# Kernel optimization log

Hardware: AMD Instinct MI355X
Metric: run time of the kernel (lower is better)

Reference implementation:

```python
import jax, jax.numpy as jnp
import numpy as np

IMG = 640
STRIDES = (8, 16, 32)
A = 5            # anchors per level
NC = 80          # num classes
IOU_TH = 0.5
NEG_RATIO = 1.0


def make_priors():
    scales = [1.0, 1.5, 2.0, 2.5, 3.0]
    out = []
    for s in STRIDES:
        f = IMG // s
        ys, xs = np.meshgrid(np.arange(f), np.arange(f), indexing='ij')
        cx = ((xs + 0.5) / f).ravel()
        cy = ((ys + 0.5) / f).ravel()
        for sc in scales:  # anchor-major to match merge_features (A, h, w) order
            wh = min(sc * 4.0 * s / IMG, 1.0)
            out.append(np.stack([cx, cy, np.full_like(cx, wh), np.full_like(cx, wh)], 1))
    return np.concatenate(out, 0).astype(np.float32)  # [42000, 4] cxcywh


def merge_features(feats):
    outs = []
    for feat in feats:
        n, c, h, w = feat.shape
        f = feat.reshape(n, A, c // A, h, w).transpose(0, 1, 3, 4, 2)
        outs.append(f.reshape(n, A * h * w, c // A))
    return jnp.concatenate(outs, axis=1)  # [n, M, 85]


def box_iou_cxcywh(a, b):
    # a [T,4], b [M,4] (cx,cy,w,h) -> IoU [T,M]
    a1 = jnp.concatenate([a[:, :2] - a[:, 2:] / 2, a[:, :2] + a[:, 2:] / 2], -1)
    b1 = jnp.concatenate([b[:, :2] - b[:, 2:] / 2, b[:, :2] + b[:, 2:] / 2], -1)
    tl = jnp.maximum(a1[:, None, :2], b1[None, :, :2])
    br = jnp.minimum(a1[:, None, 2:], b1[None, :, 2:])
    wh = jnp.clip(br - tl, 0.0)
    inter = wh[..., 0] * wh[..., 1]
    area_a = a[:, 2] * a[:, 3]
    area_b = b[:, 2] * b[:, 3]
    return inter / (area_a[:, None] + area_b[None, :] - inter + 1e-9)


def build_targets(targets, priors, batch):
    ious = box_iou_cxcywh(targets[:, 2:6], priors)  # [Nt, M]
    Nt, M = ious.shape
    img_ids = targets[:, 0].astype(jnp.int32)

    def per_image(i):
        valid = img_ids == i  # [Nt]
        iv = jnp.where(valid[:, None], ious, -1.0)
        best_gt_overlap = iv.max(0)            # [M]
        best_gt_idx = iv.argmax(0)             # [M]
        best_prior_idx = iv.argmax(1)          # [Nt]
        # torch: index_fill_(1) then sequential best_gt_overlap[best_prior_idx[j]] = j
        local_j = (jnp.cumsum(valid.astype(jnp.int32)) - 1).astype(jnp.float32)
        scat_idx = jnp.where(valid, best_prior_idx, M)  # drop invalid rows
        best_gt_overlap = best_gt_overlap.at[scat_idx].set(local_j, mode='drop')
        bbox = targets[best_gt_idx, 2:6]
        clss = targets[best_gt_idx, 1] + 1.0
        clss = jnp.where(best_gt_overlap < IOU_TH, 0.0, clss)
        t_xy = (bbox[:, :2] - priors[:, :2]) / priors[:, 2:]
        t_wh = jnp.log(bbox[:, 2:] / priors[:, 2:])
        return t_xy, t_wh, clss

    return jax.vmap(per_image)(jnp.arange(batch))  # [B,M,2],[B,M,2],[B,M]


def _smooth_l1(x):
    ax = jnp.abs(x)
    return jnp.where(ax < 1.0, 0.5 * ax * ax, ax - 0.5)


def compute_loss(preds, priors, targets):
    n, m, _ = preds.shape
    t_xy, t_wh, t_cls = build_targets(targets, priors, n)
    pos = t_cls > 0
    posf = pos.astype(preds.dtype)
    num_pos = posf.sum()

    # lbox: smooth L1 on xy and wh over positives (mean over pos*2 elements each)
    den2 = jnp.maximum(num_pos * 2.0, 1.0)
    lbox = (_smooth_l1(preds[..., 0:2] - t_xy) * posf[..., None]).sum() / den2 \
         + (_smooth_l1(preds[..., 2:4] - t_wh) * posf[..., None]).sum() / den2

    # lcls: cross entropy over positives, labels = t_cls - 1
    labels = jnp.clip(t_cls.astype(jnp.int32) - 1, 0, NC - 1)
    logz = jax.nn.log_softmax(preds[..., 5:], axis=-1)
    ce = -jnp.take_along_axis(logz, labels[..., None], axis=-1)[..., 0]
    lcls = (ce * posf).sum() / jnp.maximum(num_pos, 1.0)

    # hard negative mining (no grad): double argsort rank trick
    obj = preds[..., 4]
    loss_c = jax.lax.stop_gradient(-jax.nn.log_sigmoid(obj))
    loss_c = jnp.where(pos, 0.0, loss_c)
    order = jnp.argsort(-loss_c, axis=-1)
    rank = jnp.argsort(order, axis=-1)
    num_neg = jnp.minimum(NEG_RATIO * num_pos, m - num_pos)
    neg = rank.astype(preds.dtype) < num_neg
    sel = (pos | neg).astype(preds.dtype)

    # lobj: BCE-with-logits over pos|neg
    z = posf
    bce = jnp.maximum(obj, 0.0) - obj * z + jnp.log1p(jnp.exp(-jnp.abs(obj)))
    lobj = (bce * sel).sum() / jnp.maximum(sel.sum(), 1.0)

    loss = lbox + lcls + lobj
    return jnp.stack([loss, lbox, lobj, lcls])


def setup_inputs() -> dict:
    key = jax.random.key(0)
    ks = jax.random.split(key, 6)
    feat0 = jax.random.normal(ks[0], (8, 425, 80, 80), jnp.float32)
    feat1 = jax.random.normal(ks[1], (8, 425, 40, 40), jnp.float32)
    feat2 = jax.random.normal(ks[2], (8, 425, 20, 20), jnp.float32)
    B, T = 8, 20
    img = jnp.repeat(jnp.arange(B, dtype=jnp.float32), T)
    cls = jax.random.randint(ks[3], (B * T,), 0, NC).astype(jnp.float32)
    cxcy = jax.random.uniform(ks[4], (B * T, 2), minval=0.2, maxval=0.8)
    wh = jax.random.uniform(ks[5], (B * T, 2), minval=0.05, maxval=0.3)
    targets = jnp.concatenate([img[:, None], cls[:, None], cxcy, wh], 1)
    priors = jnp.asarray(make_priors())
    return {"feat0": feat0, "feat1": feat1, "feat2": feat2,
            "targets": targets, "priors": priors}


def reference(feat0, feat1, feat2, targets, priors):
    preds = merge_features([feat0, feat1, feat2])  # [8, 42000, 85]
    return compute_loss(preds, priors, targets)    # [loss, lbox, lobj, lcls]
```

## Files before the change

### kernel.cpp

```cpp
#include <hip/hip_runtime.h>
#include <math.h>

#define MTOT 42000
#define NB 8
#define NCLS 80
#define CAP_LIST 4096
#define MAXT 256
#define NT_MAX 2048
#define GX_MAIN 165
#define NBLK_MAIN (GX_MAIN*NB)
#define NCH 32
#define CS 1313

#define O_OVR 0
#define O_GIX (O_OVR + NB*MTOT*4)
#define O_OBJ (O_GIX + NB*MTOT*4)
#define O_LSC (O_OBJ + NB*MTOT*4)
#define O_BCE (O_LSC + NB*MTOT*4)
#define O_LST (O_BCE + NB*MTOT*4)
#define O_LJ  (O_LST + NB*MAXT*4)
#define O_CNT (O_LJ + NT_MAX*4)
#define O_BPP (((O_CNT + 64 + 7)/8)*8)
#define O_PA  (O_BPP + NT_MAX*NCH*8)
#define O_PN  (O_PA + NBLK_MAIN*16)
#define O_P2  (O_PN + NBLK_MAIN*4)
#define O_BINL (O_P2 + NBLK_MAIN*8)
#define O_HA  (((O_BINL + NB*CAP_LIST*2*4 + 255)/256)*256)
#define O_HB  (O_HA + NB*256*4)
#define O_ACC (O_HB + NB*256*4)
#define O_ACCI (O_ACC + 64)
#define O_ZEND (O_ACCI + 128)
#define ZWORDS ((O_ZEND - O_HA)/4)
#define ZBLK ((ZWORDS + 255)/256)

__device__ __forceinline__ float iou_cxcywh(float acx,float acy,float aw,float ah,
                                            float bcx,float bcy,float bw,float bh){
  float ax0=acx-aw*0.5f, ay0=acy-ah*0.5f, ax1=acx+aw*0.5f, ay1=acy+ah*0.5f;
  float bx0=bcx-bw*0.5f, by0=bcy-bh*0.5f, bx1=bcx+bw*0.5f, by1=bcy+bh*0.5f;
  float tlx=fmaxf(ax0,bx0), tly=fmaxf(ay0,by0);
  float brx=fminf(ax1,bx1), bry=fminf(ay1,by1);
  float wx=fmaxf(brx-tlx,0.f), wy=fmaxf(bry-tly,0.f);
  float inter=wx*wy;
  return inter/(aw*ah+bw*bh-inter+1e-9f);
}

__device__ __forceinline__ float sl1(float x){
  float ax=fabsf(x); return ax<1.f ? 0.5f*ax*ax : ax-0.5f;
}

__device__ __forceinline__ void feat_base(const float* f0,const float* f1,const float* f2,
                                          int i,int m,const float** basep,int* hwp){
  const float* fp; int hw, loc;
  if(m<32000){ fp=f0; hw=6400; loc=m; }
  else if(m<40000){ fp=f1; hw=1600; loc=m-32000; }
  else { fp=f2; hw=400; loc=m-40000; }
  int a=loc/hw, p=loc-a*hw;
  *basep = fp + (size_t)(i*425 + a*85)*(size_t)hw + p;
  *hwp = hw;
}

__device__ __forceinline__ void fine_scan(const unsigned* hb,int ca,int kres,int* bs_out,int* r_out){
  if(ca==0x7fffffff){ *bs_out=0x7fffffff; *r_out=0; return; }
  int run=0, bs=-1, r=0;
  for(int f=255;f>=0;f--){
    int cb=(int)hb[f];
    if(run<kres && run+cb>=kres){ bs=(ca<<8)|f; r=kres-run; break; }
    run+=cb;
  }
  if(bs<0){ bs=(ca<<8); r=kres-run; }
  *bs_out=bs; *r_out=r;
}

__global__ void k_init(const float* __restrict__ tg, int nt, int* __restrict__ list,
                       int* __restrict__ cnt, int* __restrict__ lj,
                       unsigned* __restrict__ zbase){
  int bx=blockIdx.x, tid=threadIdx.x;
  if(bx<ZBLK){
    int w=bx*256+tid;
    if(w<ZWORDS) zbase[w]=0u;
    return;
  }
  if(bx==ZBLK && tid<NB){
    int c=0;
    for(int q=0;q<nt;q++) if((int)tg[q*6]==tid) c++;
    cnt[tid]=c;
  }
  int t=(bx-ZBLK)*256+tid;
  if(t>=nt) return;
  int img=(int)tg[t*6];
  int j=0;
  for(int q=0;q<t;q++) if((int)tg[q*6]==img) j++;
  lj[t]=j;
  if(img>=0 && img<NB && j<MAXT) list[img*MAXT+j]=t;
}

__global__ void k_big1(const float* __restrict__ f0,const float* __restrict__ f1,const float* __restrict__ f2,
                       const float* __restrict__ tg,const float* __restrict__ priors,
                       const int* __restrict__ list,const int* __restrict__ cnt,int nt,
                       float* __restrict__ ovr,int* __restrict__ gix,
                       float* __restrict__ objc,unsigned long long* __restrict__ bpp){
  __shared__ float st[MAXT*6];
  __shared__ int sidx[MAXT];
  __shared__ unsigned long long su[256];
  int b=blockIdx.x, tid=threadIdx.x;
  if(b<NBLK_MAIN){
    int i=b/GX_MAIN, cb=b-(b/GX_MAIN)*GX_MAIN;
    int n=min(cnt[i],MAXT);
    for(int j=tid;j<n;j+=256){
      int t=list[i*MAXT+j];
      sidx[j]=t;
      #pragma unroll
      for(int q=0;q<6;q++) st[j*6+q]=tg[t*6+q];
    }
    __syncthreads();
    int m=cb*256+tid;
    if(m>=MTOT) return;
    float4 pr=((const float4*)priors)[m];
    float maxv=-1.f; int bi=0;
    for(int j=0;j<n;j++){
      float v=iou_cxcywh(st[j*6+2],st[j*6+3],st[j*6+4],st[j*6+5],pr.x,pr.y,pr.z,pr.w);
      if(v>maxv){ maxv=v; bi=sidx[j]; }
    }
    ovr[i*MTOT+m]=maxv; gix[i*MTOT+m]=bi;
  } else if(b<2*NBLK_MAIN){
    int idx=b-NBLK_MAIN;
    int i=idx/GX_MAIN, cb=idx-(idx/GX_MAIN)*GX_MAIN;
    int m=cb*256+tid;
    if(m>=MTOT) return;
    const float* base; int hw;
    feat_base(f0,f1,f2,i,m,&base,&hw);
    objc[i*MTOT+m]=base[(size_t)4*hw];
  } else {
    int idx=b-2*NBLK_MAIN;
    int t=idx/NCH, c=idx-(idx/NCH)*NCH;
    float acx=tg[t*6+2],acy=tg[t*6+3],aw=tg[t*6+4],ah=tg[t*6+5];
    int m0=c*CS, m1=min(m0+CS,MTOT);
    float bv=-1.f; int bm=0;
    for(int m=m0+tid;m<m1;m+=256){
      float4 pr=((const float4*)priors)[m];
      float v=iou_cxcywh(acx,acy,aw,ah,pr.x,pr.y,pr.z,pr.w);
      if(v>bv){ bv=v; bm=m; }
    }
    unsigned long long p=(bv<0.f)?0ull
        :(((unsigned long long)__float_as_uint(bv))<<32)|(unsigned)(~bm);
    su[tid]=p;
    __syncthreads();
    for(int o=128;o>0;o>>=1){
      if(tid<o){ if(su[tid+o]>su[tid]) su[tid]=su[tid+o]; }
      __syncthreads();
    }
    if(tid==0) bpp[(size_t)t*NCH+c]=su[0];
  }
}

__global__ void k_bpsc(const float* __restrict__ tg,int nt,
                       const unsigned long long* __restrict__ bpp,
                       const int* __restrict__ lj,float* __restrict__ ovr){
  __shared__ int tbp[NT_MAX];
  __shared__ int timg[NT_MAX];
  int tid=threadIdx.x;
  for(int t=tid;t<nt;t+=256){
    unsigned long long best=0ull;
    const unsigned long long* pp=&bpp[(size_t)t*NCH];
    for(int c=0;c<NCH;c++){ unsigned long long v=pp[c]; if(v>best) best=v; }
    int bm=~((unsigned)(best&0xFFFFFFFFull));
    tbp[t]=min(max(bm,0),MTOT-1);
    timg[t]=(int)tg[t*6];
  }
  __syncthreads();
  for(int t=tid;t<nt;t+=256){
    int img=timg[t];
    if(img<0||img>=NB) continue;
    int myp=tbp[t];
    bool last=true;
    for(int q=t+1;q<nt;q++) if(timg[q]==img&&tbp[q]==myp){ last=false; break; }
    if(last) ovr[img*MTOT+myp]=(float)lj[t];
  }
}

__global__ void k_lc(const float* __restrict__ tg,const float* __restrict__ objc,
                     const float* __restrict__ ovr,const int* __restrict__ gix,int nt,
                     float* __restrict__ lsc,float* __restrict__ bcearr,
                     unsigned* __restrict__ histA,int* __restrict__ partN){
  __shared__ unsigned h[256];
  __shared__ int snp[4];
  int tid=threadIdx.x, lane=tid&63, wid=tid>>6;
  h[tid]=0u;
  __syncthreads();
  int i=blockIdx.y;
  int m=blockIdx.x*256+tid;
  int npos=0;
  if(m<MTOT){
    int gid=i*MTOT+m;
    float ov=ovr[gid];
    int gi=min(max(gix[gid],0),nt-1);
    float tc=tg[gi*6+1]+1.f;
    bool pos=(ov>=0.5f)&&(tc>0.f);
    float obj=objc[gid];
    float sp=log1pf(expf(-fabsf(obj)));
    float bce=fmaxf(obj,0.f)-(pos?obj:0.f)+sp;
    float lc=pos?0.f:(fmaxf(-obj,0.f)+sp);
    lsc[gid]=lc; bcearr[gid]=bce;
    atomicAdd(&h[__float_as_uint(lc)>>24],1u);
    npos=pos?1:0;
  }
  #pragma unroll
  for(int o=32;o>0;o>>=1) npos+=__shfl_xor(npos,o);
  if(lane==0) snp[wid]=npos;
  __syncthreads();
  unsigned hc=h[tid];
  if(hc) atomicAdd(&histA[i*256+tid],hc);
  if(tid==0) partN[blockIdx.y*GX_MAIN+blockIdx.x]=snp[0]+snp[1]+snp[2]+snp[3];
}

__global__ void k_redscanA(const int* __restrict__ partN,const unsigned* __restrict__ histA,
                           int* __restrict__ acci){
  __shared__ int an[256];
  __shared__ unsigned h[256];
  int t=threadIdx.x, b=blockIdx.x;
  int n=0;
  for(int e=t;e<NBLK_MAIN;e+=256) n+=partN[e];
  an[t]=n;
  __syncthreads();
  for(int o=128;o>0;o>>=1){ if(t<o) an[t]+=an[t+o]; __syncthreads(); }
  int np=an[0];
  if(b==0&&t==0) acci[0]=np;
  h[t]=histA[b*256+t];
  __syncthreads();
  if(t==0){
    int kk=min(np,MTOT-np);
    if(kk<=0){ acci[2+b]=0x7fffffff; acci[10+b]=0; }
    else{
      int run=0, ca=-1, kres=0;
      for(int c2=255;c2>=0;c2--){
        int cbn=(int)h[c2];
        if(run<kk&&run+cbn>=kk){ ca=c2; kres=kk-run; break; }
        run+=cbn;
      }
      if(ca<0){ ca=0; kres=kk-run; }
      acci[2+b]=ca; acci[10+b]=kres;
    }
  }
}

__global__ void k_big2(const float* __restrict__ f0,const float* __restrict__ f1,const float* __restrict__ f2,
                       const float* __restrict__ tg,const float* __restrict__ priors,
                       const float* __restrict__ ovr,const int* __restrict__ gix,
                       const float* __restrict__ lsc,const float* __restrict__ bcearr,
                       const int* __restrict__ acci,int nt,
                       unsigned* __restrict__ histB,float4* __restrict__ partA){
  __shared__ unsigned h[256];
  __shared__ float rA[4],rB[4],rC[4],rD[4];
  int b=blockIdx.x, tid=threadIdx.x, lane=tid&63, wid=tid>>6;
  if(b<NBLK_MAIN){
    h[tid]=0u;
    __syncthreads();
    int i=b/GX_MAIN, cb=b-(b/GX_MAIN)*GX_MAIN;
    int ca=acci[2+i];
    int m=cb*256+tid;
    if(m<MTOT && ca!=0x7fffffff){
      unsigned u=__float_as_uint(lsc[i*MTOT+m]);
      if((int)(u>>24)==ca) atomicAdd(&h[(u>>16)&0xFF],1u);
    }
    __syncthreads();
    unsigned c=h[tid];
    if(c) atomicAdd(&histB[i*256+tid],c);
  } else {
    int idx=b-NBLK_MAIN;
    int i=idx/GX_MAIN, cb=idx-(idx/GX_MAIN)*GX_MAIN;
    int m=cb*256+tid;
    bool valid=(m<MTOT);
    float lxy=0.f,lwh=0.f,bcep=0.f,wce=0.f;
    bool pos=false; int gi=0;
    if(valid){
      int gid=i*MTOT+m;
      float ov=ovr[gid];
      gi=min(max(gix[gid],0),nt-1);
      float tc=tg[gi*6+1]+1.f;
      pos=(ov>=0.5f)&&(tc>0.f);
      if(pos){
        const float* base; int hw;
        feat_base(f0,f1,f2,i,m,&base,&hw);
        bcep=bcearr[gid];
        float4 pr=((const float4*)priors)[m];
        float bx=tg[gi*6+2],by=tg[gi*6+3],bw=tg[gi*6+4],bh=tg[gi*6+5];
        float tx=(bx-pr.x)/pr.z, ty=(by-pr.y)/pr.w;
        float tw=logf(bw/pr.z), th=logf(bh/pr.w);
        lxy=sl1(base[0]-tx)+sl1(base[(size_t)hw]-ty);
        lwh=sl1(base[(size_t)2*hw]-tw)+sl1(base[(size_t)3*hw]-th);
      }
    }
    unsigned long long mask=__ballot(valid&&pos);
    while(mask){
      int s=__ffsll(mask)-1;
      mask&=mask-1;
      int m_s=__shfl(m,s);
      int gi_s=__shfl(gi,s);
      const float* bs2; int hws;
      feat_base(f0,f1,f2,i,m_s,&bs2,&hws);
      int label=(int)(tg[gi_s*6+1]+1.f)-1;
      label=min(NCLS-1,max(0,label));
      float v0=bs2[(size_t)(5+lane)*hws];
      float v1=(lane<16)?bs2[(size_t)(69+lane)*hws]:-3.0e38f;
      float mx=fmaxf(v0,v1);
      #pragma unroll
      for(int o=32;o>0;o>>=1) mx=fmaxf(mx,__shfl_xor(mx,o));
      float se=expf(v0-mx)+((lane<16)?expf(v1-mx):0.f);
      float xl=((lane==label)?v0:0.f)+((lane<16&&lane+64==label)?v1:0.f);
      #pragma unroll
      for(int o=32;o>0;o>>=1){ se+=__shfl_xor(se,o); xl+=__shfl_xor(xl,o); }
      wce+=logf(se)+mx-xl;
    }
    #pragma unroll
    for(int o=32;o>0;o>>=1){
      lxy+=__shfl_xor(lxy,o); lwh+=__shfl_xor(lwh,o); bcep+=__shfl_xor(bcep,o);
    }
    if(lane==0){ rA[wid]=lxy; rB[wid]=lwh; rC[wid]=wce; rD[wid]=bcep; }
    __syncthreads();
    if(tid==0)
      partA[idx]=make_float4(rA[0]+rA[1]+rA[2]+rA[3], rB[0]+rB[1]+rB[2]+rB[3],
                             rC[0]+rC[1]+rC[2]+rC[3], rD[0]+rD[1]+rD[2]+rD[3]);
  }
}

__global__ void k_select(const float* __restrict__ lsc,const float* __restrict__ bcearr,
                         const unsigned* __restrict__ histB,
                         int* __restrict__ acci,float2* __restrict__ part2,
                         int* __restrict__ binlist){
  __shared__ unsigned hb[256];
  __shared__ int sbs;
  __shared__ float ss[4]; __shared__ float sc[4];
  int tid=threadIdx.x, lane=tid&63, wid=tid>>6;
  int i=blockIdx.y;
  int ca=acci[2+i], kres=acci[10+i];
  hb[tid]=(ca==0x7fffffff)?0u:histB[i*256+tid];
  __syncthreads();
  if(tid==0){ int bs,r; fine_scan(hb,ca,kres,&bs,&r); sbs=bs; }
  __syncthreads();
  int bs_=sbs;
  int m=blockIdx.x*256+tid;
  float s=0.f, c=0.f;
  if(m<MTOT){
    int gid=i*MTOT+m;
    unsigned u=__float_as_uint(lsc[gid]);
    int bin=(int)(u>>16);
    if(bin>bs_){ s=bcearr[gid]; c=1.f; }
    else if(bin==bs_){
      int idx=atomicAdd(&acci[18+i],1);
      if(idx<CAP_LIST){
        binlist[((size_t)i*CAP_LIST+idx)*2  ]=(int)u;
        binlist[((size_t)i*CAP_LIST+idx)*2+1]=gid;
      }
    }
  }
  #pragma unroll
  for(int o=32;o>0;o>>=1){ s+=__shfl_xor(s,o); c+=__shfl_xor(c,o); }
  if(lane==0){ ss[wid]=s; sc[wid]=c; }
  __syncthreads();
  if(tid==0) part2[blockIdx.y*gridDim.x+blockIdx.x]=make_float2(ss[0]+ss[1]+ss[2]+ss[3], sc[0]+sc[1]+sc[2]+sc[3]);
}

__global__ void k_ties(const float* __restrict__ bcearr,int* __restrict__ acci,
                       float* __restrict__ accf,const int* __restrict__ binlist,
                       const unsigned* __restrict__ histB){
  __shared__ unsigned hb[256];
  __shared__ int sbs, sr;
  int i=blockIdx.x, tid=threadIdx.x;
  int ca=acci[2+i], kres=acci[10+i];
  hb[tid]=(ca==0x7fffffff)?0u:histB[i*256+tid];
  __syncthreads();
  if(tid==0){ int bs,r; fine_scan(hb,ca,kres,&bs,&r); sbs=bs; sr=r; }
  __syncthreads();
  if(sbs==0x7fffffff) return;
  int n=min(acci[18+i],CAP_LIST);
  int r=sr;
  for(int e=tid;e<n;e+=blockDim.x){
    unsigned ue=(unsigned)binlist[((size_t)i*CAP_LIST+e)*2];
    int ge=binlist[((size_t)i*CAP_LIST+e)*2+1];
    int rank=0;
    for(int q=0;q<n;q++){
      unsigned uq=(unsigned)binlist[((size_t)i*CAP_LIST+q)*2];
      int gq=binlist[((size_t)i*CAP_LIST+q)*2+1];
      rank += ((uq>ue)||(uq==ue&&gq<ge))?1:0;
    }
    if(rank<r){
      atomicAdd(&accf[5], bcearr[ge]);
      atomicAdd(&acci[1], 1);
    }
  }
}

__global__ void k_final(const float4* __restrict__ partA,const float2* __restrict__ part2,
                        const float* __restrict__ accf,const int* __restrict__ acci,
                        float* __restrict__ out){
  __shared__ float a0[256],a1[256],a2[256],a3[256],s0[256],s1[256];
  int tid=threadIdx.x;
  float x=0,y=0,z=0,w=0,ns=0,nc=0;
  for(int e=tid;e<NBLK_MAIN;e+=256){
    float4 p=partA[e]; x+=p.x; y+=p.y; z+=p.z; w+=p.w;
    float2 q=part2[e]; ns+=q.x; nc+=q.y;
  }
  a0[tid]=x; a1[tid]=y; a2[tid]=z; a3[tid]=w; s0[tid]=ns; s1[tid]=nc;
  __syncthreads();
  for(int o=128;o>0;o>>=1){
    if(tid<o){
      a0[tid]+=a0[tid+o]; a1[tid]+=a1[tid+o]; a2[tid]+=a2[tid+o]; a3[tid]+=a3[tid+o];
      s0[tid]+=s0[tid+o]; s1[tid]+=s1[tid+o];
    }
    __syncthreads();
  }
  if(tid==0){
    float negsum=s0[0]+accf[5];
    float negcnt=s1[0]+(float)acci[1];
    int np=acci[0];
    float npf=(float)np;
    float den2=fmaxf(2.f*npf,1.f);
    float lbox=a0[0]/den2+a1[0]/den2;
    float lcls=a2[0]/fmaxf(npf,1.f);
    float selc=npf+negcnt;
    float lobj=(a3[0]+negsum)/fmaxf(selc,1.f);
    out[0]=lbox+lcls+lobj;
    out[1]=lbox;
    out[2]=lobj;
    out[3]=lcls;
  }
}

extern "C" void kernel_launch(void* const* d_in, const int* in_sizes, int n_in,
                              void* d_out, int out_size, void* d_ws, size_t ws_size,
                              hipStream_t stream) {
  const float* f0=(const float*)d_in[0];
  const float* f1=(const float*)d_in[1];
  const float* f2=(const float*)d_in[2];
  const float* tg=(const float*)d_in[3];
  const float* priors=(const float*)d_in[4];
  int nt = in_sizes[3]/6;
  if(nt>NT_MAX) nt=NT_MAX;
  if(nt<1) nt=1;

  char* ws=(char*)d_ws;
  float*    ovr    =(float*)   (ws+O_OVR);
  int*      gix    =(int*)     (ws+O_GIX);
  float*    objc   =(float*)   (ws+O_OBJ);
  float*    lsc    =(float*)   (ws+O_LSC);
  float*    bcearr =(float*)   (ws+O_BCE);
  int*      list   =(int*)     (ws+O_LST);
  int*      lj     =(int*)     (ws+O_LJ);
  int*      cnt    =(int*)     (ws+O_CNT);
  unsigned long long* bpp=(unsigned long long*)(ws+O_BPP);
  float4*   partA  =(float4*)  (ws+O_PA);
  int*      partN  =(int*)     (ws+O_PN);
  float2*   part2  =(float2*)  (ws+O_P2);
  int*      binlist=(int*)     (ws+O_BINL);
  unsigned* histA  =(unsigned*)(ws+O_HA);
  unsigned* histB  =(unsigned*)(ws+O_HB);
  float*    accf   =(float*)   (ws+O_ACC);
  int*      acci   =(int*)     (ws+O_ACCI);
  unsigned* zbase  =(unsigned*)(ws+O_HA);

  int ntb=(nt+255)/256;
  k_init<<<ZBLK+ntb,256,0,stream>>>(tg,nt,list,cnt,lj,zbase);
  k_big1<<<2*NBLK_MAIN+nt*NCH,256,0,stream>>>(f0,f1,f2,tg,priors,list,cnt,nt,ovr,gix,objc,bpp);
  k_bpsc<<<1,256,0,stream>>>(tg,nt,bpp,lj,ovr);
  dim3 gm(GX_MAIN, NB);
  k_lc<<<gm,256,0,stream>>>(tg,objc,ovr,gix,nt,lsc,bcearr,histA,partN);
  k_redscanA<<<NB,256,0,stream>>>(partN,histA,acci);
  k_big2<<<2*NBLK_MAIN,256,0,stream>>>(f0,f1,f2,tg,priors,ovr,gix,lsc,bcearr,acci,nt,histB,partA);
  k_select<<<gm,256,0,stream>>>(lsc,bcearr,histB,acci,part2,binlist);
  k_ties<<<NB,256,0,stream>>>(bcearr,acci,accf,binlist,histB);
  k_final<<<1,256,0,stream>>>(partA,part2,accf,acci,(float*)d_out);
}
```

Before: 138.3 us.

## Fuse init into main IoU kernel, filter targets by image inline, stage tie list in LDS

Merges the init kernel (zeroing, per-target local index) into the big matching kernel, which removes one launch and the per-image list/count dependency. Each prior-matching block now scans all targets in shared-memory chunks and skips targets from other images. The best-prior search uses 8 larger chunks per target instead of 32, giving fewer blocks but more work each. k_ties stages up to 2048 bin-list entries in LDS so the O(n^2) rank loop reads shared memory instead of global memory. The trade-off is that every prior block now iterates over all targets rather than only its image's targets.

```diff
diff --git a/kernel.cpp b/kernel.cpp
--- a/kernel.cpp
+++ b/kernel.cpp
@@ -9,19 +9,18 @@
 #define NT_MAX 2048
 #define GX_MAIN 165
 #define NBLK_MAIN (GX_MAIN*NB)
-#define NCH 32
-#define CS 1313
+#define NCHB 8
+#define CSB 5250
+#define TCH 512
 
 #define O_OVR 0
 #define O_GIX (O_OVR + NB*MTOT*4)
 #define O_OBJ (O_GIX + NB*MTOT*4)
 #define O_LSC (O_OBJ + NB*MTOT*4)
 #define O_BCE (O_LSC + NB*MTOT*4)
-#define O_LST (O_BCE + NB*MTOT*4)
-#define O_LJ  (O_LST + NB*MAXT*4)
-#define O_CNT (O_LJ + NT_MAX*4)
-#define O_BPP (((O_CNT + 64 + 7)/8)*8)
-#define O_PA  (O_BPP + NT_MAX*NCH*8)
+#define O_LJ  (O_BCE + NB*MTOT*4)
+#define O_BPP (((O_LJ + NT_MAX*4 + 7)/8)*8)
+#define O_PA  (O_BPP + NT_MAX*NCHB*8)
 #define O_PN  (O_PA + NBLK_MAIN*16)
 #define O_P2  (O_PN + NBLK_MAIN*4)
 #define O_BINL (O_P2 + NBLK_MAIN*8)
@@ -71,59 +70,56 @@
   *bs_out=bs; *r_out=r;
 }
 
-__global__ void k_init(const float* __restrict__ tg, int nt, int* __restrict__ list,
-                       int* __restrict__ cnt, int* __restrict__ lj,
-                       unsigned* __restrict__ zbase){
-  int bx=blockIdx.x, tid=threadIdx.x;
-  if(bx<ZBLK){
-    int w=bx*256+tid;
+__global__ void k_big0(const float* __restrict__ f0,const float* __restrict__ f1,const float* __restrict__ f2,
+                       const float* __restrict__ tg,const float* __restrict__ priors,
+                       int nt,int b0,int b1,int b2,
+                       int* __restrict__ lj,unsigned* __restrict__ zbase,
+                       float* __restrict__ ovr,int* __restrict__ gix,
+                       float* __restrict__ objc,unsigned long long* __restrict__ bpp){
+  __shared__ float st[TCH*6];
+  __shared__ unsigned long long su[256];
+  int b=blockIdx.x, tid=threadIdx.x;
+  if(b<ZBLK){
+    int w=b*256+tid;
     if(w<ZWORDS) zbase[w]=0u;
     return;
   }
-  if(bx==ZBLK && tid<NB){
-    int c=0;
-    for(int q=0;q<nt;q++) if((int)tg[q*6]==tid) c++;
-    cnt[tid]=c;
-  }
-  int t=(bx-ZBLK)*256+tid;
-  if(t>=nt) return;
-  int img=(int)tg[t*6];
-  int j=0;
-  for(int q=0;q<t;q++) if((int)tg[q*6]==img) j++;
-  lj[t]=j;
-  if(img>=0 && img<NB && j<MAXT) list[img*MAXT+j]=t;
-}
-
-__global__ void k_big1(const float* __restrict__ f0,const float* __restrict__ f1,const float* __restrict__ f2,
-                       const float* __restrict__ tg,const float* __restrict__ priors,
-                       const int* __restrict__ list,const int* __restrict__ cnt,int nt,
-                       float* __restrict__ ovr,int* __restrict__ gix,
-                       float* __restrict__ objc,unsigned long long* __restrict__ bpp){
-  __shared__ float st[MAXT*6];
-  __shared__ int sidx[MAXT];
-  __shared__ unsigned long long su[256];
-  int b=blockIdx.x, tid=threadIdx.x;
-  if(b<NBLK_MAIN){
-    int i=b/GX_MAIN, cb=b-(b/GX_MAIN)*GX_MAIN;
-    int n=min(cnt[i],MAXT);
-    for(int j=tid;j<n;j+=256){
-      int t=list[i*MAXT+j];
-      sidx[j]=t;
-      #pragma unroll
-      for(int q=0;q<6;q++) st[j*6+q]=tg[t*6+q];
-    }
-    __syncthreads();
+  if(b<b0){
+    int t=(b-ZBLK)*256+tid;
+    if(t>=nt) return;
+    int img=(int)tg[t*6];
+    int j=0;
+    for(int q=0;q<t;q++) if((int)tg[q*6]==img) j++;
+    lj[t]=j;
+    return;
+  }
+  if(b<b1){
+    int idx=b-b0;
+    int i=idx/GX_MAIN, cb=idx-(idx/GX_MAIN)*GX_MAIN;
     int m=cb*256+tid;
-    if(m>=MTOT) return;
-    float4 pr=((const float4*)priors)[m];
+    bool valid=(m<MTOT);
+    float4 pr=make_float4(0.f,0.f,1.f,1.f);
+    if(valid) pr=((const float4*)priors)[m];
     float maxv=-1.f; int bi=0;
-    for(int j=0;j<n;j++){
-      float v=iou_cxcywh(st[j*6+2],st[j*6+3],st[j*6+4],st[j*6+5],pr.x,pr.y,pr.z,pr.w);
-      if(v>maxv){ maxv=v; bi=sidx[j]; }
-    }
-    ovr[i*MTOT+m]=maxv; gix[i*MTOT+m]=bi;
-  } else if(b<2*NBLK_MAIN){
-    int idx=b-NBLK_MAIN;
+    for(int base=0;base<nt;base+=TCH){
+      int nch=min(TCH,nt-base);
+      for(int j=tid;j<nch;j+=256){
+        #pragma unroll
+        for(int q=0;q<6;q++) st[j*6+q]=tg[(base+j)*6+q];
+      }
+      __syncthreads();
+      if(valid){
+        for(int j=0;j<nch;j++){
+          if((int)st[j*6]!=i) continue;
+          float v=iou_cxcywh(st[j*6+2],st[j*6+3],st[j*6+4],st[j*6+5],pr.x,pr.y,pr.z,pr.w);
+          if(v>maxv){ maxv=v; bi=base+j; }
+        }
+      }
+      __syncthreads();
+    }
+    if(valid){ ovr[i*MTOT+m]=maxv; gix[i*MTOT+m]=bi; }
+  } else if(b<b2){
+    int idx=b-b1;
     int i=idx/GX_MAIN, cb=idx-(idx/GX_MAIN)*GX_MAIN;
     int m=cb*256+tid;
     if(m>=MTOT) return;
@@ -131,10 +127,10 @@
     feat_base(f0,f1,f2,i,m,&base,&hw);
     objc[i*MTOT+m]=base[(size_t)4*hw];
   } else {
-    int idx=b-2*NBLK_MAIN;
-    int t=idx/NCH, c=idx-(idx/NCH)*NCH;
+    int idx=b-b2;
+    int t=idx/NCHB, c=idx-(idx/NCHB)*NCHB;
     float acx=tg[t*6+2],acy=tg[t*6+3],aw=tg[t*6+4],ah=tg[t*6+5];
-    int m0=c*CS, m1=min(m0+CS,MTOT);
+    int m0=c*CSB, m1=min(m0+CSB,MTOT);
     float bv=-1.f; int bm=0;
     for(int m=m0+tid;m<m1;m+=256){
       float4 pr=((const float4*)priors)[m];
@@ -149,7 +145,7 @@
       if(tid<o){ if(su[tid+o]>su[tid]) su[tid]=su[tid+o]; }
       __syncthreads();
     }
-    if(tid==0) bpp[(size_t)t*NCH+c]=su[0];
+    if(tid==0) bpp[(size_t)t*NCHB+c]=su[0];
   }
 }
 
@@ -161,8 +157,9 @@
   int tid=threadIdx.x;
   for(int t=tid;t<nt;t+=256){
     unsigned long long best=0ull;
-    const unsigned long long* pp=&bpp[(size_t)t*NCH];
-    for(int c=0;c<NCH;c++){ unsigned long long v=pp[c]; if(v>best) best=v; }
+    const unsigned long long* pp=&bpp[(size_t)t*NCHB];
+    #pragma unroll
+    for(int c=0;c<NCHB;c++){ unsigned long long v=pp[c]; if(v>best) best=v; }
     int bm=~((unsigned)(best&0xFFFFFFFFull));
     tbp[t]=min(max(bm,0),MTOT-1);
     timg[t]=(int)tg[t*6];
@@ -360,11 +357,13 @@
   if(tid==0) part2[blockIdx.y*gridDim.x+blockIdx.x]=make_float2(ss[0]+ss[1]+ss[2]+ss[3], sc[0]+sc[1]+sc[2]+sc[3]);
 }
 
+#define TSTAGE 2048
 __global__ void k_ties(const float* __restrict__ bcearr,int* __restrict__ acci,
                        float* __restrict__ accf,const int* __restrict__ binlist,
                        const unsigned* __restrict__ histB){
   __shared__ unsigned hb[256];
   __shared__ int sbs, sr;
+  __shared__ int sl[TSTAGE*2];
   int i=blockIdx.x, tid=threadIdx.x;
   int ca=acci[2+i], kres=acci[10+i];
   hb[tid]=(ca==0x7fffffff)?0u:histB[i*256+tid];
@@ -373,14 +372,22 @@
   __syncthreads();
   if(sbs==0x7fffffff) return;
   int n=min(acci[18+i],CAP_LIST);
+  int nstage=min(n,TSTAGE);
+  for(int e=tid;e<nstage;e+=256){
+    sl[e*2  ]=binlist[((size_t)i*CAP_LIST+e)*2  ];
+    sl[e*2+1]=binlist[((size_t)i*CAP_LIST+e)*2+1];
+  }
+  __syncthreads();
   int r=sr;
   for(int e=tid;e<n;e+=blockDim.x){
-    unsigned ue=(unsigned)binlist[((size_t)i*CAP_LIST+e)*2];
-    int ge=binlist[((size_t)i*CAP_LIST+e)*2+1];
+    unsigned ue; int ge;
+    if(e<nstage){ ue=(unsigned)sl[e*2]; ge=sl[e*2+1]; }
+    else{ ue=(unsigned)binlist[((size_t)i*CAP_LIST+e)*2]; ge=binlist[((size_t)i*CAP_LIST+e)*2+1]; }
     int rank=0;
     for(int q=0;q<n;q++){
-      unsigned uq=(unsigned)binlist[((size_t)i*CAP_LIST+q)*2];
-      int gq=binlist[((size_t)i*CAP_LIST+q)*2+1];
+      unsigned uq; int gq;
+      if(q<nstage){ uq=(unsigned)sl[q*2]; gq=sl[q*2+1]; }
+      else{ uq=(unsigned)binlist[((size_t)i*CAP_LIST+q)*2]; gq=binlist[((size_t)i*CAP_LIST+q)*2+1]; }
       rank += ((uq>ue)||(uq==ue&&gq<ge))?1:0;
     }
     if(rank<r){
@@ -444,9 +451,7 @@
   float*    objc   =(float*)   (ws+O_OBJ);
   float*    lsc    =(float*)   (ws+O_LSC);
   float*    bcearr =(float*)   (ws+O_BCE);
-  int*      list   =(int*)     (ws+O_LST);
   int*      lj     =(int*)     (ws+O_LJ);
-  int*      cnt    =(int*)     (ws+O_CNT);
   unsigned long long* bpp=(unsigned long long*)(ws+O_BPP);
   float4*   partA  =(float4*)  (ws+O_PA);
   int*      partN  =(int*)     (ws+O_PN);
@@ -459,8 +464,8 @@
   unsigned* zbase  =(unsigned*)(ws+O_HA);
 
   int ntb=(nt+255)/256;
-  k_init<<<ZBLK+ntb,256,0,stream>>>(tg,nt,list,cnt,lj,zbase);
-  k_big1<<<2*NBLK_MAIN+nt*NCH,256,0,stream>>>(f0,f1,f2,tg,priors,list,cnt,nt,ovr,gix,objc,bpp);
+  int b0=ZBLK+ntb, b1=b0+NBLK_MAIN, b2=b1+NBLK_MAIN;
+  k_big0<<<b2+nt*NCHB,256,0,stream>>>(f0,f1,f2,tg,priors,nt,b0,b1,b2,lj,zbase,ovr,gix,objc,bpp);
   k_bpsc<<<1,256,0,stream>>>(tg,nt,bpp,lj,ovr);
   dim3 gm(GX_MAIN, NB);
   k_lc<<<gm,256,0,stream>>>(tg,objc,ovr,gix,nt,lsc,bcearr,histA,partN);
```

New measurement: 132.9 us. 1.04x faster.
